# Kernel optimization log

Hardware: AMD Instinct MI355X
Metric: run time of the kernel (lower is better)

Reference implementation:

```python
import jax, jax.numpy as jnp
import numpy as np

N, IN, OUT = 1024, 256, 256

def setup_inputs() -> dict:
    key = jax.random.key(0)
    ks = jax.random.split(key, 8)
    hl = jax.random.normal(ks[0], (N, IN), jnp.float32)
    # hr >= hl so (hl, hr) is a valid interval input
    hr = hl + jax.random.uniform(ks[1], (N, IN), jnp.float32)
    u = lambda k, shape: jax.random.uniform(k, shape, jnp.float32, 0.02, 0.05)  # matches reset_parameters init
    w_b = u(ks[2], (IN, OUT))
    w_a = u(ks[3], (IN, OUT))
    w_c = u(ks[4], (IN, OUT))
    b_b = u(ks[5], (1, OUT))
    b_a = u(ks[6], (1, OUT))
    b_c = u(ks[7], (1, OUT))
    return {"hl": hl, "hr": hr, "w_b": w_b, "w_a": w_a, "w_c": w_c, "b_b": b_b, "b_a": b_a, "b_c": b_c}

def reference(hl, hr, w_b, w_a, w_c, b_b, b_a, b_c):
    # limit_parameters: relu on the spread parameters
    w_a = jax.nn.relu(w_a)
    w_c = jax.nn.relu(w_c)
    b_a = jax.nn.relu(b_a)
    b_c = jax.nn.relu(b_c)
    # interval weight / bias endpoints
    w_l = w_b - w_a  # [IN, OUT]
    w_r = w_b + w_c
    b_l = b_b - b_a  # [1, OUT]
    b_r = b_b + b_c
    # interval matmul: per (n,k,j) take min/max of 4 endpoint products, sum over k.
    # (Equivalent to torch interval_prod's expand/reshape/stack/min/max/sum.)
    xl = hl[:, :, None]  # [N, IN, 1]
    xr = hr[:, :, None]
    p1 = xl * w_l[None]  # [N, IN, OUT]
    p2 = xl * w_r[None]
    p3 = xr * w_l[None]
    p4 = xr * w_r[None]
    out_l = jnp.sum(jnp.minimum(jnp.minimum(p1, p2), jnp.minimum(p3, p4)), axis=1) + b_l
    out_r = jnp.sum(jnp.maximum(jnp.maximum(p1, p2), jnp.maximum(p3, p4)), axis=1) + b_r
    return (out_l, out_r)
```

## Files before the change

### kernel.cpp

```cpp
#include <hip/hip_runtime.h>

#define NN    1024
#define IN_D  256
#define OUT_D 256
#define BN    4
#define NI2   (IN_D / 2)
#define KH2   (NI2 / 2)

typedef float v2f __attribute__((ext_vector_type(2)));
typedef float v4f __attribute__((ext_vector_type(4)));

#define WLR_BYTES (sizeof(float4) * NI2 * OUT_D)

__global__ __launch_bounds__(256) void fz_prep(
    const float* __restrict__ wb, const float* __restrict__ wa,
    const float* __restrict__ wc, float4* __restrict__ wlr2) {
    int t = blockIdx.x * 256 + threadIdx.x;
    int ii2 = t >> 8;
    int o   = t & (OUT_D - 1);
    int i0  = (2 * ii2) * OUT_D + o;
    int i1  = i0 + OUT_D;
    float4 w;
    w.x = wb[i0] - fmaxf(wa[i0], 0.0f);
    w.y = wb[i0] + fmaxf(wc[i0], 0.0f);
    w.z = wb[i1] - fmaxf(wa[i1], 0.0f);
    w.w = wb[i1] + fmaxf(wc[i1], 0.0f);
    wlr2[t] = w;
}

template <bool PREP>
__global__ __launch_bounds__(512) void fz_main(
    const float* __restrict__ hl, const float* __restrict__ hr,
    const float* __restrict__ wb, const float* __restrict__ wa,
    const float* __restrict__ wc, const float4* __restrict__ wlr2,
    const float* __restrict__ bb, const float* __restrict__ ba,
    const float* __restrict__ bc, float* __restrict__ out) {
    __shared__ __align__(16) v2f ab[BN][IN_D];
    __shared__ __align__(16) v2f pl[BN][OUT_D];

    const int o  = threadIdx.x & (OUT_D - 1);
    const int h  = threadIdx.x >> 8;
    const int n0 = blockIdx.x * BN;

    for (int p = threadIdx.x; p < BN * IN_D; p += 512) {
        int tn = p >> 8;
        int ii = p & (IN_D - 1);
        v2f v; v.x = hl[(n0 + tn) * IN_D + ii];
        v.y = hr[(n0 + tn) * IN_D + ii];
        ab[tn][ii] = v;
    }
    __syncthreads();

    v2f slr[BN];
#pragma unroll
    for (int t = 0; t < BN; ++t) { slr[t].x = 0.0f; slr[t].y = 0.0f; }

    const float4* wp = wlr2 + (size_t)(h * KH2) * OUT_D + o;

#pragma unroll 4
    for (int j = 0; j < KH2; ++j) {
        float4 w;
        if (PREP) {
            w = wp[(size_t)j * OUT_D];
        } else {
            int i0 = (h * KH2 + j) * 2 * OUT_D + o;
            int i1 = i0 + OUT_D;
            w.x = wb[i0] - fmaxf(wa[i0], 0.0f);
            w.y = wb[i0] + fmaxf(wc[i0], 0.0f);
            w.z = wb[i1] - fmaxf(wa[i1], 0.0f);
            w.w = wb[i1] + fmaxf(wc[i1], 0.0f);
        }
        const int ii = (h * KH2 + j) * 2;
#pragma unroll
        for (int t = 0; t < BN; ++t) {
            v4f a4 = *reinterpret_cast<const v4f*>(&ab[t][ii]);
            v2f ab0; ab0.x = a4.x; ab0.y = a4.y;
            v2f l0 = ab0 * w.x;
            v2f r0 = ab0 * w.y;
            v2f mm0;
            mm0.x = fminf(fminf(l0.x, l0.y), r0.x);
            mm0.y = fmaxf(fmaxf(l0.x, l0.y), r0.y);
            slr[t] += mm0;
            v2f ab1; ab1.x = a4.z; ab1.y = a4.w;
            v2f l1 = ab1 * w.z;
            v2f r1 = ab1 * w.w;
            v2f mm1;
            mm1.x = fminf(fminf(l1.x, l1.y), r1.x);
            mm1.y = fmaxf(fmaxf(l1.x, l1.y), r1.y);
            slr[t] += mm1;
        }
    }

    if (h == 1) {
#pragma unroll
        for (int t = 0; t < BN; ++t) pl[t][o] = slr[t];
    }
    __syncthreads();
    if (h == 0) {
        float bv = bb[o];
        float bl = bv - fmaxf(ba[o], 0.0f);
        float br = bv + fmaxf(bc[o], 0.0f);
#pragma unroll
        for (int t = 0; t < BN; ++t) {
            v2f s = slr[t];
            v2f q = pl[t][o];
            out[(n0 + t) * OUT_D + o]              = s.x + q.x + bl;
            out[NN * OUT_D + (n0 + t) * OUT_D + o] = s.y + q.y + br;
        }
    }
}

extern "C" void kernel_launch(void* const* d_in, const int* in_sizes, int n_in,
                              void* d_out, int out_size, void* d_ws, size_t ws_size,
                              hipStream_t stream) {
    const float* hl = (const float*)d_in[0];
    const float* hr = (const float*)d_in[1];
    const float* wb = (const float*)d_in[2];
    const float* wa = (const float*)d_in[3];
    const float* wc = (const float*)d_in[4];
    const float* bb = (const float*)d_in[5];
    const float* ba = (const float*)d_in[6];
    const float* bc = (const float*)d_in[7];
    float* out = (float*)d_out;

    dim3 grid(NN / BN);

    if (ws_size >= WLR_BYTES) {
        float4* wlr2 = (float4*)d_ws;
        fz_prep<<<(NI2 * OUT_D) / 256, 256, 0, stream>>>(wb, wa, wc, wlr2);
        fz_main<true><<<grid, 512, 0, stream>>>(hl, hr, wb, wa, wc, wlr2,
                                                bb, ba, bc, out);
    } else {
        fz_main<false><<<grid, 512, 0, stream>>>(hl, hr, wb, wa, wc, nullptr,
                                                 bb, ba, bc, out);
    }
}
```

Baseline: 25.74 us.

## Split K over eight thread groups with two outputs per thread

The main kernel now launches 1024 threads per block. The input dimension is split across 8 groups instead of 2, and each thread computes two output columns (oslot and oslot+128), so every thread keeps 4 rows × 2 outputs of accumulators. Partial sums from 7 groups pass through a larger shared-memory buffer and group 0 reduces them. The aim is a shorter serial K loop per thread and more in-flight weight loads. In exchange it adds a bigger cross-group reduction, more LDS traffic, and possibly lower occupancy from larger blocks.

```diff
diff --git a/kernel.cpp b/kernel.cpp
--- a/kernel.cpp
+++ b/kernel.cpp
@@ -1,11 +1,13 @@
 #include <hip/hip_runtime.h>
 
-#define NN    1024
-#define IN_D  256
-#define OUT_D 256
-#define BN    4
-#define NI2   (IN_D / 2)
-#define KH2   (NI2 / 2)
+#define NN     1024
+#define IN_D   256
+#define OUT_D  256
+#define BN     4
+#define NI2    (IN_D / 2)
+#define NG     8
+#define JPG    (NI2 / NG)
+#define OSLOTS (OUT_D / 2)
 
 typedef float v2f __attribute__((ext_vector_type(2)));
 typedef float v4f __attribute__((ext_vector_type(4)));
@@ -29,83 +31,120 @@
 }
 
 template <bool PREP>
-__global__ __launch_bounds__(512) void fz_main(
+__global__ __launch_bounds__(1024) void fz_main(
     const float* __restrict__ hl, const float* __restrict__ hr,
     const float* __restrict__ wb, const float* __restrict__ wa,
     const float* __restrict__ wc, const float4* __restrict__ wlr2,
     const float* __restrict__ bb, const float* __restrict__ ba,
     const float* __restrict__ bc, float* __restrict__ out) {
     __shared__ __align__(16) v2f ab[BN][IN_D];
-    __shared__ __align__(16) v2f pl[BN][OUT_D];
+    __shared__ __align__(16) v2f pl[NG - 1][BN][2][OSLOTS];
 
-    const int o  = threadIdx.x & (OUT_D - 1);
-    const int h  = threadIdx.x >> 8;
-    const int n0 = blockIdx.x * BN;
+    const int tid   = threadIdx.x;
+    const int oslot = tid & (OSLOTS - 1);
+    const int g     = tid >> 7;
+    const int n0    = blockIdx.x * BN;
 
-    for (int p = threadIdx.x; p < BN * IN_D; p += 512) {
-        int tn = p >> 8;
-        int ii = p & (IN_D - 1);
-        v2f v; v.x = hl[(n0 + tn) * IN_D + ii];
-        v.y = hr[(n0 + tn) * IN_D + ii];
-        ab[tn][ii] = v;
+    {
+        int row = tid >> 8;
+        int ii  = tid & (IN_D - 1);
+        v2f v; v.x = hl[(n0 + row) * IN_D + ii];
+        v.y = hr[(n0 + row) * IN_D + ii];
+        ab[row][ii] = v;
     }
     __syncthreads();
 
-    v2f slr[BN];
+    v2f acc[BN][2];
 #pragma unroll
-    for (int t = 0; t < BN; ++t) { slr[t].x = 0.0f; slr[t].y = 0.0f; }
+    for (int t = 0; t < BN; ++t) {
+        acc[t][0].x = 0.0f; acc[t][0].y = 0.0f;
+        acc[t][1].x = 0.0f; acc[t][1].y = 0.0f;
+    }
 
-    const float4* wp = wlr2 + (size_t)(h * KH2) * OUT_D + o;
+    const int j0 = g * JPG;
+    const float4* wp0 = wlr2 + (size_t)j0 * OUT_D + oslot;
+    const float4* wp1 = wp0 + OSLOTS;
 
 #pragma unroll 4
-    for (int j = 0; j < KH2; ++j) {
-        float4 w;
+    for (int j = 0; j < JPG; ++j) {
+        float4 w0, w1;
         if (PREP) {
-            w = wp[(size_t)j * OUT_D];
+            w0 = wp0[(size_t)j * OUT_D];
+            w1 = wp1[(size_t)j * OUT_D];
         } else {
-            int i0 = (h * KH2 + j) * 2 * OUT_D + o;
-            int i1 = i0 + OUT_D;
-            w.x = wb[i0] - fmaxf(wa[i0], 0.0f);
-            w.y = wb[i0] + fmaxf(wc[i0], 0.0f);
-            w.z = wb[i1] - fmaxf(wa[i1], 0.0f);
-            w.w = wb[i1] + fmaxf(wc[i1], 0.0f);
+            int base = (j0 + j) * 2 * OUT_D;
+            int i00 = base + oslot, i01 = i00 + OUT_D;
+            w0.x = wb[i00] - fmaxf(wa[i00], 0.0f);
+            w0.y = wb[i00] + fmaxf(wc[i00], 0.0f);
+            w0.z = wb[i01] - fmaxf(wa[i01], 0.0f);
+            w0.w = wb[i01] + fmaxf(wc[i01], 0.0f);
+            int i10 = base + oslot + OSLOTS, i11 = i10 + OUT_D;
+            w1.x = wb[i10] - fmaxf(wa[i10], 0.0f);
+            w1.y = wb[i10] + fmaxf(wc[i10], 0.0f);
+            w1.z = wb[i11] - fmaxf(wa[i11], 0.0f);
+            w1.w = wb[i11] + fmaxf(wc[i11], 0.0f);
         }
-        const int ii = (h * KH2 + j) * 2;
+        const int ii = (j0 + j) * 2;
 #pragma unroll
         for (int t = 0; t < BN; ++t) {
             v4f a4 = *reinterpret_cast<const v4f*>(&ab[t][ii]);
-            v2f ab0; ab0.x = a4.x; ab0.y = a4.y;
-            v2f l0 = ab0 * w.x;
-            v2f r0 = ab0 * w.y;
-            v2f mm0;
-            mm0.x = fminf(fminf(l0.x, l0.y), r0.x);
-            mm0.y = fmaxf(fmaxf(l0.x, l0.y), r0.y);
-            slr[t] += mm0;
-            v2f ab1; ab1.x = a4.z; ab1.y = a4.w;
-            v2f l1 = ab1 * w.z;
-            v2f r1 = ab1 * w.w;
-            v2f mm1;
-            mm1.x = fminf(fminf(l1.x, l1.y), r1.x);
-            mm1.y = fmaxf(fmaxf(l1.x, l1.y), r1.y);
-            slr[t] += mm1;
+            v2f p0; p0.x = a4.x; p0.y = a4.y;
+            v2f p1; p1.x = a4.z; p1.y = a4.w;
+            {
+                v2f l = p0 * w0.x, r = p0 * w0.y;
+                v2f mm; mm.x = fminf(fminf(l.x, l.y), r.x);
+                mm.y = fmaxf(fmaxf(l.x, l.y), r.y);
+                acc[t][0] += mm;
+            }
+            {
+                v2f l = p1 * w0.z, r = p1 * w0.w;
+                v2f mm; mm.x = fminf(fminf(l.x, l.y), r.x);
+                mm.y = fmaxf(fmaxf(l.x, l.y), r.y);
+                acc[t][0] += mm;
+            }
+            {
+                v2f l = p0 * w1.x, r = p0 * w1.y;
+                v2f mm; mm.x = fminf(fminf(l.x, l.y), r.x);
+                mm.y = fmaxf(fmaxf(l.x, l.y), r.y);
+                acc[t][1] += mm;
+            }
+            {
+                v2f l = p1 * w1.z, r = p1 * w1.w;
+                v2f mm; mm.x = fminf(fminf(l.x, l.y), r.x);
+                mm.y = fmaxf(fmaxf(l.x, l.y), r.y);
+                acc[t][1] += mm;
+            }
         }
     }
 
-    if (h == 1) {
+    if (g > 0) {
 #pragma unroll
-        for (int t = 0; t < BN; ++t) pl[t][o] = slr[t];
+        for (int t = 0; t < BN; ++t) {
+            pl[g - 1][t][0][oslot] = acc[t][0];
+            pl[g - 1][t][1][oslot] = acc[t][1];
+        }
     }
     __syncthreads();
-    if (h == 0) {
-        float bv = bb[o];
-        float bl = bv - fmaxf(ba[o], 0.0f);
-        float br = bv + fmaxf(bc[o], 0.0f);
+    if (g == 0) {
+        const int o0 = oslot, o1 = oslot + OSLOTS;
+        float bl0 = bb[o0] - fmaxf(ba[o0], 0.0f);
+        float br0 = bb[o0] + fmaxf(bc[o0], 0.0f);
+        float bl1 = bb[o1] - fmaxf(ba[o1], 0.0f);
+        float br1 = bb[o1] + fmaxf(bc[o1], 0.0f);
 #pragma unroll
         for (int t = 0; t < BN; ++t) {
-            v2f s = slr[t];
-            v2f q = pl[t][o];
-            out[(n0 + t) * OUT_D + o]              = s.x + q.x + bl;
-            out[NN * OUT_D + (n0 + t) * OUT_D + o] = s.y + q.y + br;
+            v2f s0 = acc[t][0], s1 = acc[t][1];
+#pragma unroll
+            for (int gg = 0; gg < NG - 1; ++gg) {
+                s0 += pl[gg][t][0][oslot];
+                s1 += pl[gg][t][1][oslot];
+            }
+            size_t rl = (size_t)(n0 + t) * OUT_D;
+            size_t rr = (size_t)NN * OUT_D + rl;
+            out[rl + o0] = s0.x + bl0;
+            out[rr + o0] = s0.y + br0;
+            out[rl + o1] = s1.x + bl1;
+            out[rr + o1] = s1.y + br1;
         }
     }
 }
@@ -128,10 +167,10 @@
     if (ws_size >= WLR_BYTES) {
         float4* wlr2 = (float4*)d_ws;
         fz_prep<<<(NI2 * OUT_D) / 256, 256, 0, stream>>>(wb, wa, wc, wlr2);
-        fz_main<true><<<grid, 512, 0, stream>>>(hl, hr, wb, wa, wc, wlr2,
-                                                bb, ba, bc, out);
+        fz_main<true><<<grid, 1024, 0, stream>>>(hl, hr, wb, wa, wc, wlr2,
+                                                 bb, ba, bc, out);
     } else {
-        fz_main<false><<<grid, 512, 0, stream>>>(hl, hr, wb, wa, wc, nullptr,
-                                                 bb, ba, bc, out);
+        fz_main<false><<<grid, 1024, 0, stream>>>(hl, hr, wb, wa, wc, nullptr,
+                                                  bb, ba, bc, out);
     }
 }
```

New measurement: 25.54 us. About the same (-0.8%).
